# Kernel tuning notes

Hardware: AMD Instinct MI355X
Metric: run time of the kernel (lower is better)

The kernel has to match this reference:

```python
import jax, jax.numpy as jnp
import numpy as np

BETA = 0.25
N_CODES = 1024
CODE_DIM = 64


def setup_inputs() -> dict:
    key = jax.random.key(0)
    k1, k2 = jax.random.split(key)
    z_e = jax.random.normal(k1, (32, CODE_DIM, 2048), dtype=jnp.float32)
    # nn.init.uniform_(weight, -1/n_codes, 1/n_codes)
    lim = 1.0 / N_CODES
    codebook = jax.random.uniform(k2, (N_CODES, CODE_DIM), dtype=jnp.float32,
                                  minval=-lim, maxval=lim)
    return {"z_e": z_e, "codebook": codebook}


def reference(z_e, codebook):
    B, C, K = z_e.shape
    # (B, C, K) -> (B*K, C)
    z = jnp.transpose(z_e, (0, 2, 1)).reshape(-1, C)
    # squared L2 distances: ||z||^2 + ||e||^2 - 2 z.e  -> (N, n_codes)
    dist = (jnp.sum(z * z, axis=1, keepdims=True)
            + jnp.sum(codebook * codebook, axis=1)[None, :]
            - 2.0 * (z @ codebook.T))
    codes = jnp.argmin(dist, axis=1)  # (N,)
    # gather quantized vectors, back to (B, C, K)
    z_q = jnp.transpose(codebook[codes].reshape(B, K, C), (0, 2, 1))
    # straight-through
    z_q_st = z_e + jax.lax.stop_gradient(z_q - z_e)
    sg = jax.lax.stop_gradient
    loss_codebook = jnp.mean((z_q - sg(z_e)) ** 2)
    loss_commit = jnp.mean((z_e - sg(z_q)) ** 2)
    loss_vq = loss_codebook + BETA * loss_commit
    # perplexity via histogram (equivalent to onehot.mean(0))
    n = codes.shape[0]
    avg_probs = jnp.zeros((N_CODES,), dtype=jnp.float32).at[codes].add(1.0) / n
    perplexity = jnp.exp(-jnp.sum(avg_probs * jnp.log(avg_probs + 1e-10)))
    return z_q_st, codes.reshape(B, K), loss_vq, perplexity
```

## Files before the change

### kernel.cpp

```cpp
#include <hip/hip_runtime.h>
#include <math.h>

#define NB 32
#define NC 64
#define NK 2048
#define NCODES 1024
#define NVEC (NB*NK)
#define NELEM (NB*NC*NK)
#define NBLK (NVEC/64)

#define MARGIN 1.5e-3f
#define CAP 32

#define WS_HIST  0
#define WS_CBN32 4096
#define WS_PART  8192
#define WS_CBBF  32768

typedef __bf16 bf16x8 __attribute__((ext_vector_type(8)));
typedef float  f32x4  __attribute__((ext_vector_type(4)));
#define MFMA16(A, B, ACC) __builtin_amdgcn_mfma_f32_16x16x32_bf16(A, B, ACC, 0, 0, 0)

__global__ void k_cbprep(const float* __restrict__ cb, float* __restrict__ n32,
                         __bf16* __restrict__ cbbf, int* __restrict__ hist) {
    const int t = threadIdx.x;
    const int j = blockIdx.x * 64 + t;
    if (blockIdx.x == 0) {
        int4 z4; z4.x = 0; z4.y = 0; z4.z = 0; z4.w = 0;
#pragma unroll
        for (int i = 0; i < 4; i++) ((int4*)hist)[t * 4 + i] = z4;
    }
    const float* cr = cb + (size_t)j * NC;
    float x[64];
#pragma unroll
    for (int i = 0; i < 16; i++) {
        f32x4 tv = *(const f32x4*)(cr + 4 * i);
        x[4*i+0] = tv[0]; x[4*i+1] = tv[1]; x[4*i+2] = tv[2]; x[4*i+3] = tv[3];
    }
    float r[8];
#pragma unroll
    for (int q = 0; q < 8; q++) r[q] = __fmul_rn(x[q], x[q]);
#pragma unroll
    for (int i = 8; i < 64; i += 8)
#pragma unroll
        for (int q = 0; q < 8; q++)
            r[q] = __fadd_rn(r[q], __fmul_rn(x[i + q], x[i + q]));
    float s01 = __fadd_rn(r[0], r[1]), s23 = __fadd_rn(r[2], r[3]);
    float s45 = __fadd_rn(r[4], r[5]), s67 = __fadd_rn(r[6], r[7]);
    n32[j] = __fadd_rn(__fadd_rn(s01, s23), __fadd_rn(s45, s67));
    __bf16* br = cbbf + (size_t)j * NC;
#pragma unroll
    for (int i = 0; i < 8; i++) {
        bf16x8 o;
#pragma unroll
        for (int q = 0; q < 8; q++) o[q] = (__bf16)x[8*i + q];
        *(bf16x8*)(br + 8*i) = o;
    }
}

__launch_bounds__(256, 4)
__global__ void k_vq(const float* __restrict__ ze, const float* __restrict__ cb,
                     const float* __restrict__ n32, const __bf16* __restrict__ cbbf,
                     int* __restrict__ hist, float* __restrict__ codes_f,
                     float* __restrict__ outq, double* __restrict__ part) {
    __shared__ float wmin[64][5];
    __shared__ float gthr[64];
    __shared__ int cnt[64];
    __shared__ int cand[64][CAP + 1];
    __shared__ unsigned long long keys2[64][5];
    __shared__ int codearr[64];
    __shared__ double lsd[4];

    const int t = threadIdx.x;
    const int L = t & 63;
    const int w = t >> 6;
    const int quad = L >> 4;
    const int col = L & 15;
    const int vec0 = blockIdx.x * 64;
    const int b = vec0 >> 11;
    const int k0 = vec0 & (NK - 1);
    const float* zbase = ze + (size_t)b * NC * NK + k0;

    bf16x8 af[4][2];
#pragma unroll
    for (int vt = 0; vt < 4; vt++)
#pragma unroll
        for (int kt = 0; kt < 2; kt++)
#pragma unroll
            for (int j = 0; j < 8; j++)
                af[vt][kt][j] =
                    (__bf16)zbase[(size_t)(kt*32 + quad*8 + j) * NK + vt*16 + col];

    float pmin[4][4];
#pragma unroll
    for (int vt = 0; vt < 4; vt++)
#pragma unroll
        for (int r = 0; r < 4; r++) pmin[vt][r] = 1e30f;
#pragma unroll 4
    for (int tile = 0; tile < 16; tile++) {
        const __bf16* brow = cbbf + (size_t)(w*256 + tile*16 + col) * NC + quad*8;
        bf16x8 b0 = *(const bf16x8*)(brow);
        bf16x8 b1 = *(const bf16x8*)(brow + 32);
        float nvv = n32[w*256 + tile*16 + col];
#pragma unroll
        for (int vt = 0; vt < 4; vt++) {
            f32x4 acc = {0.f, 0.f, 0.f, 0.f};
            acc = MFMA16(af[vt][0], b0, acc);
            acc = MFMA16(af[vt][1], b1, acc);
#pragma unroll
            for (int r = 0; r < 4; r++) {
                float pd = __fmaf_rn(-2.f, acc[r], nvv);
                pmin[vt][r] = fminf(pmin[vt][r], pd);
            }
        }
    }
#pragma unroll
    for (int vt = 0; vt < 4; vt++)
#pragma unroll
        for (int r = 0; r < 4; r++) {
            float pm = pmin[vt][r];
            pm = fminf(pm, __shfl_xor(pm, 1, 16));
            pm = fminf(pm, __shfl_xor(pm, 2, 16));
            pm = fminf(pm, __shfl_xor(pm, 4, 16));
            pm = fminf(pm, __shfl_xor(pm, 8, 16));
            if (col == 0) wmin[vt*16 + quad*4 + r][w] = pm;
        }
    __syncthreads();

    if (t < 64) {
        float g = wmin[t][0];
#pragma unroll
        for (int ww = 1; ww < 4; ww++) g = fminf(g, wmin[t][ww]);
        gthr[t] = g + MARGIN;
        cnt[t] = 0;
    }
    __syncthreads();

    float thr[4][4];
#pragma unroll
    for (int vt = 0; vt < 4; vt++)
#pragma unroll
        for (int r = 0; r < 4; r++) thr[vt][r] = gthr[vt*16 + quad*4 + r];
#pragma unroll 4
    for (int tile = 0; tile < 16; tile++) {
        const __bf16* brow = cbbf + (size_t)(w*256 + tile*16 + col) * NC + quad*8;
        bf16x8 b0 = *(const bf16x8*)(brow);
        bf16x8 b1 = *(const bf16x8*)(brow + 32);
        float nvv = n32[w*256 + tile*16 + col];
#pragma unroll
        for (int vt = 0; vt < 4; vt++) {
            f32x4 acc = {0.f, 0.f, 0.f, 0.f};
            acc = MFMA16(af[vt][0], b0, acc);
            acc = MFMA16(af[vt][1], b1, acc);
#pragma unroll
            for (int r = 0; r < 4; r++) {
                float pd = __fmaf_rn(-2.f, acc[r], nvv);
                if (pd <= thr[vt][r]) {
                    int m = vt*16 + quad*4 + r;
                    int slot = atomicAdd(&cnt[m], 1);
                    if (slot < CAP) cand[m][slot] = w*256 + tile*16 + col;
                }
            }
        }
    }
    __syncthreads();

    {
        const int v = L;
        float rr[8];
#pragma unroll
        for (int q = 0; q < 8; q++) {
            float xx = zbase[(size_t)q * NK + v];
            rr[q] = __fmul_rn(xx, xx);
        }
#pragma unroll
        for (int i = 8; i < 64; i += 8)
#pragma unroll
            for (int q = 0; q < 8; q++) {
                float xx = zbase[(size_t)(i + q) * NK + v];
                rr[q] = __fadd_rn(rr[q], __fmul_rn(xx, xx));
            }
        float s01 = __fadd_rn(rr[0], rr[1]), s23 = __fadd_rn(rr[2], rr[3]);
        float s45 = __fadd_rn(rr[4], rr[5]), s67 = __fadd_rn(rr[6], rr[7]);
        float t1 = __fadd_rn(__fadd_rn(s01, s23), __fadd_rn(s45, s67));

        int cc = cnt[v];
        unsigned long long kmin = 0xFFFFFFFFFFFFFFFFULL;
        if (cc <= CAP) {
            for (int si = w; si < cc; si += 4) {
                int j = cand[v][si];
                const float* cr = cb + (size_t)j * NC;
                float a = 0.f;
#pragma unroll
                for (int c = 0; c < NC; c++)
                    a = __fmaf_rn(zbase[(size_t)c * NK + v], cr[c], a);
                float d = __fmaf_rn(-2.f, a, __fadd_rn(t1, n32[j]));
                unsigned long long key =
                    ((unsigned long long)__float_as_uint(d) << 32) | (unsigned int)j;
                if (key < kmin) kmin = key;
            }
        } else {
            for (int j = w * 256; j < (w + 1) * 256; j++) {
                const float* cr = cb + (size_t)j * NC;
                float a = 0.f;
#pragma unroll
                for (int c = 0; c < NC; c++)
                    a = __fmaf_rn(zbase[(size_t)c * NK + v], cr[c], a);
                float d = __fmaf_rn(-2.f, a, __fadd_rn(t1, n32[j]));
                unsigned long long key =
                    ((unsigned long long)__float_as_uint(d) << 32) | (unsigned int)j;
                if (key < kmin) kmin = key;
            }
        }
        keys2[v][w] = kmin;
    }
    __syncthreads();

    if (t < 64) {
        unsigned long long kmin = keys2[t][0];
#pragma unroll
        for (int ww = 1; ww < 4; ww++) {
            unsigned long long kk = keys2[t][ww];
            if (kk < kmin) kmin = kk;
        }
        int code = (int)(kmin & 0xFFFFFFFFu);
        codearr[t] = code;
        codes_f[vec0 + t] = (float)code;
        atomicAdd(&hist[code], 1);
    }
    __syncthreads();

    double s = 0.0;
    float* ob = outq + (size_t)b * NC * NK + k0;
    const int c0 = t >> 4;
    const int v0 = (t & 15) * 4;
    int cds[4];
#pragma unroll
    for (int u = 0; u < 4; u++) cds[u] = codearr[v0 + u];
#pragma unroll
    for (int half = 0; half < 4; half++) {
        const int c = c0 + half * 16;
        f32x4 zv = *(const f32x4*)(zbase + (size_t)c * NK + v0);
        f32x4 ov;
#pragma unroll
        for (int u = 0; u < 4; u++) {
            float qv = cb[(size_t)cds[u] * NC + c];
            ov[u] = __fadd_rn(zv[u], __fsub_rn(qv, zv[u]));
            double d = (double)qv - (double)zv[u];
            s += d * d;
        }
        *(f32x4*)(ob + (size_t)c * NK + v0) = ov;
    }
    for (int off = 32; off; off >>= 1) s += __shfl_down(s, off);
    if (L == 0) lsd[w] = s;
    __syncthreads();
    if (t == 0) part[blockIdx.x] = lsd[0] + lsd[1] + lsd[2] + lsd[3];
}

__launch_bounds__(1024)
__global__ void k_final(const double* __restrict__ part, const int* __restrict__ hist,
                        float* __restrict__ out) {
    int t = threadIdx.x;
    double vL = part[t];
    double p = (double)hist[t] * (1.0 / (double)NVEC);
    double vE = p * log(p + 1e-10);
    for (int off = 32; off; off >>= 1) {
        vL += __shfl_down(vL, off);
        vE += __shfl_down(vE, off);
    }
    __shared__ double lsL[16], lsE[16];
    int lane = t & 63, wv = t >> 6;
    if (lane == 0) { lsL[wv] = vL; lsE[wv] = vE; }
    __syncthreads();
    if (t == 0) {
        double SL = 0.0, SE = 0.0;
        for (int i = 0; i < 16; i++) { SL += lsL[i]; SE += lsE[i]; }
        double loss_cb = SL / (double)NELEM;
        out[NELEM + NVEC]     = (float)(loss_cb + 0.25 * loss_cb);
        out[NELEM + NVEC + 1] = (float)exp(-SE);
    }
}

extern "C" void kernel_launch(void* const* d_in, const int* in_sizes, int n_in,
                              void* d_out, int out_size, void* d_ws, size_t ws_size,
                              hipStream_t stream) {
    const float* ze = (const float*)d_in[0];
    const float* cb = (const float*)d_in[1];
    float* out = (float*)d_out;
    char* ws = (char*)d_ws;

    int*    hist = (int*)(ws + WS_HIST);
    float*  n32  = (float*)(ws + WS_CBN32);
    double* part = (double*)(ws + WS_PART);
    __bf16* cbbf = (__bf16*)(ws + WS_CBBF);

    float* zq      = out;
    float* codes_f = out + NELEM;

    k_cbprep<<<16, 64, 0, stream>>>(cb, n32, cbbf, hist);
    k_vq<<<NBLK, 256, 0, stream>>>(ze, cb, n32, cbbf, hist, codes_f, zq, part);
    k_final<<<1, 1024, 0, stream>>>(part, hist, out);
}
```

Measured before the change: 128.0 us.

## Track top-2 per lane in first pass to skip candidate rescan

The first distance pass now keeps, per lane, the best and second-best distances plus the best code index. Candidates are taken from the lane-local minimum directly. The second full MFMA pass over the codebook runs only when some lane's second-best also falls within the margin threshold, and then only for the vectors that need it. This is meant to avoid recomputing the full distance matrix in most blocks, at the cost of extra registers and select instructions in the hot loop, which may lower occupancy.

```diff
diff --git a/kernel.cpp b/kernel.cpp
--- a/kernel.cpp
+++ b/kernel.cpp
@@ -66,6 +66,8 @@
     __shared__ float wmin[64][5];
     __shared__ float gthr[64];
     __shared__ int cnt[64];
+    __shared__ int needv[64];
+    __shared__ int blockneed;
     __shared__ int cand[64][CAP + 1];
     __shared__ unsigned long long keys2[64][5];
     __shared__ int codearr[64];
@@ -91,17 +93,21 @@
                 af[vt][kt][j] =
                     (__bf16)zbase[(size_t)(kt*32 + quad*8 + j) * NK + vt*16 + col];
 
-    float pmin[4][4];
+    float m1[4][4], m2[4][4];
+    int   i1[4][4];
 #pragma unroll
     for (int vt = 0; vt < 4; vt++)
 #pragma unroll
-        for (int r = 0; r < 4; r++) pmin[vt][r] = 1e30f;
+        for (int r = 0; r < 4; r++) {
+            m1[vt][r] = 1e30f; m2[vt][r] = 1e30f; i1[vt][r] = 0;
+        }
 #pragma unroll 4
     for (int tile = 0; tile < 16; tile++) {
         const __bf16* brow = cbbf + (size_t)(w*256 + tile*16 + col) * NC + quad*8;
         bf16x8 b0 = *(const bf16x8*)(brow);
         bf16x8 b1 = *(const bf16x8*)(brow + 32);
         float nvv = n32[w*256 + tile*16 + col];
+        const int code = w*256 + tile*16 + col;
 #pragma unroll
         for (int vt = 0; vt < 4; vt++) {
             f32x4 acc = {0.f, 0.f, 0.f, 0.f};
@@ -110,7 +116,11 @@
 #pragma unroll
             for (int r = 0; r < 4; r++) {
                 float pd = __fmaf_rn(-2.f, acc[r], nvv);
-                pmin[vt][r] = fminf(pmin[vt][r], pd);
+                bool lt = pd < m1[vt][r];
+                float nm2 = fminf(m2[vt][r], pd);
+                m2[vt][r] = lt ? m1[vt][r] : nm2;
+                i1[vt][r] = lt ? code : i1[vt][r];
+                m1[vt][r] = lt ? pd : m1[vt][r];
             }
         }
     }
@@ -118,7 +128,7 @@
     for (int vt = 0; vt < 4; vt++)
 #pragma unroll
         for (int r = 0; r < 4; r++) {
-            float pm = pmin[vt][r];
+            float pm = m1[vt][r];
             pm = fminf(pm, __shfl_xor(pm, 1, 16));
             pm = fminf(pm, __shfl_xor(pm, 2, 16));
             pm = fminf(pm, __shfl_xor(pm, 4, 16));
@@ -133,37 +143,54 @@
         for (int ww = 1; ww < 4; ww++) g = fminf(g, wmin[t][ww]);
         gthr[t] = g + MARGIN;
         cnt[t] = 0;
-    }
-    __syncthreads();
-
-    float thr[4][4];
+        needv[t] = 0;
+    }
+    if (t == 0) blockneed = 0;
+    __syncthreads();
+
 #pragma unroll
     for (int vt = 0; vt < 4; vt++)
 #pragma unroll
-        for (int r = 0; r < 4; r++) thr[vt][r] = gthr[vt*16 + quad*4 + r];
+        for (int r = 0; r < 4; r++) {
+            const int m = vt*16 + quad*4 + r;
+            const float thr = gthr[m];
+            if (m1[vt][r] <= thr) {
+                int slot = atomicAdd(&cnt[m], 1);
+                if (slot < CAP) cand[m][slot] = i1[vt][r];
+            }
+            if (m2[vt][r] <= thr) { needv[m] = 1; blockneed = 1; }
+        }
+    __syncthreads();
+
+    if (blockneed) {
+        if (t < 64 && needv[t]) cnt[t] = 0;
+        __syncthreads();
 #pragma unroll 4
-    for (int tile = 0; tile < 16; tile++) {
-        const __bf16* brow = cbbf + (size_t)(w*256 + tile*16 + col) * NC + quad*8;
-        bf16x8 b0 = *(const bf16x8*)(brow);
-        bf16x8 b1 = *(const bf16x8*)(brow + 32);
-        float nvv = n32[w*256 + tile*16 + col];
-#pragma unroll
-        for (int vt = 0; vt < 4; vt++) {
-            f32x4 acc = {0.f, 0.f, 0.f, 0.f};
-            acc = MFMA16(af[vt][0], b0, acc);
-            acc = MFMA16(af[vt][1], b1, acc);
-#pragma unroll
-            for (int r = 0; r < 4; r++) {
-                float pd = __fmaf_rn(-2.f, acc[r], nvv);
-                if (pd <= thr[vt][r]) {
-                    int m = vt*16 + quad*4 + r;
-                    int slot = atomicAdd(&cnt[m], 1);
-                    if (slot < CAP) cand[m][slot] = w*256 + tile*16 + col;
+        for (int tile = 0; tile < 16; tile++) {
+            const __bf16* brow = cbbf + (size_t)(w*256 + tile*16 + col) * NC + quad*8;
+            bf16x8 b0 = *(const bf16x8*)(brow);
+            bf16x8 b1 = *(const bf16x8*)(brow + 32);
+            float nvv = n32[w*256 + tile*16 + col];
+#pragma unroll
+            for (int vt = 0; vt < 4; vt++) {
+                f32x4 acc = {0.f, 0.f, 0.f, 0.f};
+                acc = MFMA16(af[vt][0], b0, acc);
+                acc = MFMA16(af[vt][1], b1, acc);
+#pragma unroll
+                for (int r = 0; r < 4; r++) {
+                    const int m = vt*16 + quad*4 + r;
+                    if (needv[m]) {
+                        float pd = __fmaf_rn(-2.f, acc[r], nvv);
+                        if (pd <= gthr[m]) {
+                            int slot = atomicAdd(&cnt[m], 1);
+                            if (slot < CAP) cand[m][slot] = w*256 + tile*16 + col;
+                        }
+                    }
                 }
             }
         }
-    }
-    __syncthreads();
+        __syncthreads();
+    }
 
     {
         const int v = L;
```

New measurement: 125.4 us, median of 2. -2.0%, faster.
